# Optimization experiments

Measured on AMD Instinct MI355X. Metric: run time of the kernel, lower is better.

The kernel has to match this reference:

```python
import jax, jax.numpy as jnp
import numpy as np
from jax import lax

B = 1024          # batch_size
T = 20            # timesteps == input_timesteps
IN_DIM = 13       # data_in_dims
OUT_DIM = 9       # data_out_dims
SU = 32           # input_units == output_units (story / weight dim)
H = 32            # LowerRNN hidden_size
INFER_LR = 0.1
INFER_ITERS = 20
L2_LAMBDA = 1e-4
B1, B2, EPS = 0.9, 0.999, 1e-8  # torch.optim.Adam defaults


def _lin_init(key, fan_in, shape):
    bound = 1.0 / np.sqrt(fan_in)
    return jax.random.uniform(key, shape, jnp.float32, -bound, bound)


def setup_inputs() -> dict:
    key = jax.random.key(0)
    ks = jax.random.split(key, 20)
    return {
        "temporal_batch_input": jax.random.normal(ks[0], (T, B, IN_DIM), jnp.float32),
        "temporal_batch_output": jax.random.uniform(ks[1], (T, B, OUT_DIM), jnp.float32),
        # hypernet: 32 -> 128 -> 256 -> 256 -> 32 (ReLU between, linear out)
        "hW1": _lin_init(ks[2], SU, (SU, 128)),   "hb1": _lin_init(ks[3], SU, (128,)),
        "hW2": _lin_init(ks[4], 128, (128, 256)), "hb2": _lin_init(ks[5], 128, (256,)),
        "hW3": _lin_init(ks[6], 256, (256, 256)), "hb3": _lin_init(ks[7], 256, (256,)),
        "hW4": _lin_init(ks[8], 256, (256, SU)),  "hb4": _lin_init(ks[9], 256, (SU,)),
        # LowerRNN: tanh RNN, input 45 = cat(x:13, weights:32)
        "Wih": _lin_init(ks[10], H, (H, IN_DIM + SU)),
        "Whh": _lin_init(ks[11], H, (H, H)),
        "bih": _lin_init(ks[12], H, (H,)),
        "bhh": _lin_init(ks[13], H, (H,)),
        # decoder: Linear(32 -> 9), ReLU applied after
        "Wd": _lin_init(ks[14], H, (H, OUT_DIM)),
        "bd": _lin_init(ks[15], H, (OUT_DIM,)),
    }


def reference(temporal_batch_input, temporal_batch_output,
              hW1, hb1, hW2, hb2, hW3, hb3, hW4, hb4,
              Wih, Whh, bih, bhh, Wd, bd):
    def hyper(s):  # [B,32] -> [B,32]
        h = jax.nn.relu(s @ hW1 + hb1)
        h = jax.nn.relu(h @ hW2 + hb2)
        h = jax.nn.relu(h @ hW3 + hb3)
        return h @ hW4 + hb4

    def rnn_cell(x, h):  # torch nn.RNN tanh cell
        return jnp.tanh(x @ Wih.T + bih + h @ Whh.T + bhh)

    def infer_loss(story, x_t, y_t, hidden):
        w = hyper(story)
        h_new = rnn_cell(jnp.concatenate([x_t, w], axis=1), hidden)
        pred = jax.nn.relu(h_new @ Wd + bd)                       # [B,9]
        err = jnp.mean(jnp.sum((y_t - pred) ** 2, axis=-1))       # batch_errors
        loss = (err
                + jnp.sum(jnp.var(story, axis=0, ddof=1))         # torch.var unbiased
                + L2_LAMBDA * jnp.mean(jnp.sum(story ** 2, axis=-1)))
        return loss, h_new

    grad_fn = jax.grad(infer_loss, has_aux=True)

    def timestep(story, xy):
        # fresh Adam state + fresh hidden every outer timestep (new optimizer each call)
        x_t, y_t = xy
        def adam_iter(carry, i):
            s, m, v, h = carry
            g, h_new = grad_fn(s, x_t, y_t, h)   # hidden is detached in torch -> constant here
            t = (i + 1).astype(s.dtype)
            m = B1 * m + (1.0 - B1) * g
            v = B2 * v + (1.0 - B2) * g * g
            mhat = m / (1.0 - B1 ** t)
            vhat = v / (1.0 - B2 ** t)
            s = s - INFER_LR * mhat / (jnp.sqrt(vhat) + EPS)
            return (s, m, v, h_new), None
        z = jnp.zeros_like(story)
        h0 = jnp.zeros((story.shape[0], H), story.dtype)
        (story, _, _, _), _ = lax.scan(adam_iter, (story, z, z, h0), jnp.arange(INFER_ITERS))
        return story, None

    story0 = jnp.zeros((B, SU), jnp.float32)
    higher, _ = lax.scan(timestep, story0, (temporal_batch_input, temporal_batch_output))
    higher = lax.stop_gradient(higher)  # story is .clone().detach() in torch

    cluster_centers = jnp.mean(higher, axis=0)  # [32]
    w = hyper(higher)                           # [B,32], broadcast over T (repeat)

    def seq_step(h, x_t):
        h = rnn_cell(jnp.concatenate([x_t, w], axis=1), h)
        return h, h
    _, hs = lax.scan(seq_step, jnp.zeros((B, H), jnp.float32), temporal_batch_input)
    preds = jax.nn.relu(hs @ Wd + bd)           # [T,B,9]
    errors = jnp.mean(jnp.sum((preds - temporal_batch_output) ** 2, axis=(0, 2)))
    return errors, cluster_centers
```

## Files before the change

### kernel.cpp

```cpp
#include <hip/hip_runtime.h>

#define NB 256
#define NT 512

constexpr int BATCH = 1024;
constexpr int TSTEPS = 20;
constexpr int IND = 13;
constexpr int OD = 9;
constexpr int SU = 32;
constexpr int HID = 32;
constexpr int ITERS = 20;
constexpr float LR = 0.1f;
constexpr float AB1 = 0.9f;
constexpr float AB2 = 0.999f;
constexpr float AEPS = 1e-8f;

constexpr unsigned SPIN_CAP = 1u << 27;

constexpr size_t OFF_CNT   = 0;
constexpr size_t OFF_ERRP  = 3072;
constexpr size_t OFF_PART  = 4096;
constexpr size_t OFF_WIHT  = 69632;
constexpr size_t OFF_WHHT  = 75392;
constexpr size_t OFF_W2T   = 79488;
constexpr size_t OFF_W3T   = 210560;
constexpr size_t OFF_W4T   = 472704;
constexpr size_t WS_NEEDED = 505472;

__device__ __forceinline__ float ld_coh_f32(const float* p) {
  return __hip_atomic_load(p, __ATOMIC_RELAXED, __HIP_MEMORY_SCOPE_AGENT);
}
__device__ __forceinline__ void st_coh_f32(float* p, float v) {
  __hip_atomic_store(p, v, __ATOMIC_RELAXED, __HIP_MEMORY_SCOPE_AGENT);
}

__device__ __forceinline__ void fma4(float4& a, const float4 w, const float h) {
  a.x += w.x * h; a.y += w.y * h; a.z += w.z * h; a.w += w.w * h;
}
__device__ __forceinline__ float dot4(const float4 a, const float4 b) {
  return a.x * b.x + a.y * b.y + a.z * b.z + a.w * b.w;
}

__global__ void prep_kernel(const float* __restrict__ Wih,
                            const float* __restrict__ Whh,
                            const float* __restrict__ W2,
                            const float* __restrict__ W3,
                            const float* __restrict__ W4,
                            char* __restrict__ ws) {
  float* WihT = reinterpret_cast<float*>(ws + OFF_WIHT);
  float* WhhT = reinterpret_cast<float*>(ws + OFF_WHHT);
  float* W2T  = reinterpret_cast<float*>(ws + OFF_W2T);
  float* W3T  = reinterpret_cast<float*>(ws + OFF_W3T);
  float* W4T  = reinterpret_cast<float*>(ws + OFF_W4T);
  int tid = blockIdx.x * blockDim.x + threadIdx.x;
  int nt = gridDim.x * blockDim.x;
  for (int idx = tid; idx < 32 * 45; idx += nt) {
    int i = idx / 45, c = idx % 45;
    WihT[c * 32 + i] = Wih[idx];
  }
  for (int idx = tid; idx < 32 * 32; idx += nt) {
    int i = idx >> 5, j = idx & 31;
    WhhT[j * 32 + i] = Whh[idx];
  }
  for (int idx = tid; idx < 256 * 128; idx += nt) {
    int k = idx >> 7, j = idx & 127;
    W2T[idx] = W2[j * 256 + k];
  }
  for (int idx = tid; idx < 256 * 256; idx += nt) {
    int k = idx >> 8, j = idx & 255;
    W3T[idx] = W3[j * 256 + k];
  }
  for (int idx = tid; idx < 32 * 256; idx += nt) {
    int k = idx >> 8, j = idx & 255;
    W4T[idx] = W4[j * 32 + k];
  }
}

__global__ __launch_bounds__(NT) void emb_kernel(
    const float* __restrict__ X, const float* __restrict__ Y,
    const float* __restrict__ pW1, const float* __restrict__ pb1,
    const float* __restrict__ pW2, const float* __restrict__ pb2,
    const float* __restrict__ pW3, const float* __restrict__ pb3,
    const float* __restrict__ pW4, const float* __restrict__ pb4,
    const float* __restrict__ pWih, const float* __restrict__ pWhh,
    const float* __restrict__ pbih, const float* __restrict__ pbhh,
    const float* __restrict__ pWd, const float* __restrict__ pbd,
    char* __restrict__ ws, float* __restrict__ out) {
  const int tid = threadIdx.x;
  const int bid = blockIdx.x;
  const int row0 = bid * 4;

  unsigned* cnt  = reinterpret_cast<unsigned*>(ws + OFF_CNT);
  float* errp = reinterpret_cast<float*>(ws + OFF_ERRP);
  float* part = reinterpret_cast<float*>(ws + OFF_PART);
  const float* WihT = reinterpret_cast<const float*>(ws + OFF_WIHT);
  const float* WhhT = reinterpret_cast<const float*>(ws + OFF_WHHT);
  const float* W2T  = reinterpret_cast<const float*>(ws + OFF_W2T);
  const float* W3T  = reinterpret_cast<const float*>(ws + OFF_W3T);
  const float* W4T  = reinterpret_cast<const float*>(ws + OFF_W4T);

  __shared__ alignas(16) float s[4][SU];
  __shared__ alignas(16) float mAd[4][SU];
  __shared__ alignas(16) float vAd[4][SU];
  __shared__ alignas(16) float hOld[4][HID];
  __shared__ alignas(16) float hNew[4][HID];
  __shared__ alignas(16) float h1[4][128];
  __shared__ alignas(16) float h2[4][256];
  __shared__ alignas(16) float h3[4][256];
  __shared__ alignas(16) float wv[4][SU];
  __shared__ alignas(16) float da[4][HID];
  __shared__ alignas(16) float dwb[4][SU];
  __shared__ alignas(16) float dsb[4][SU];
  __shared__ alignas(16) float red2[8192];
  __shared__ float xs[4][IND];
  __shared__ float ysd[4][OD];
  __shared__ float dadec[4][OD];
  __shared__ float mu[SU];
  __shared__ float red[8][SU];

  auto spin_ge = [&](unsigned* cntp, unsigned tgt) {
    unsigned n = 0;
    while (__hip_atomic_load(cntp, __ATOMIC_RELAXED,
                             __HIP_MEMORY_SCOPE_AGENT) < tgt) {
      __builtin_amdgcn_s_sleep(1);
      if (++n >= SPIN_CAP) break;
    }
  };


  auto fwd_l1 = [&]() {
    if (tid < 256) {
      int j0 = (tid & 31) * 4, kg = tid >> 5;
      float4 a0 = {0,0,0,0}, a1 = a0, a2 = a0, a3 = a0;
#pragma unroll
      for (int q = 0; q < 4; ++q) {
        int k = kg * 4 + q;
        float4 w = *reinterpret_cast<const float4*>(pW1 + k * 128 + j0);
        fma4(a0, w, s[0][k]); fma4(a1, w, s[1][k]);
        fma4(a2, w, s[2][k]); fma4(a3, w, s[3][k]);
      }
      *reinterpret_cast<float4*>(&red2[(kg * 4 + 0) * 128 + j0]) = a0;
      *reinterpret_cast<float4*>(&red2[(kg * 4 + 1) * 128 + j0]) = a1;
      *reinterpret_cast<float4*>(&red2[(kg * 4 + 2) * 128 + j0]) = a2;
      *reinterpret_cast<float4*>(&red2[(kg * 4 + 3) * 128 + j0]) = a3;
    }
    __syncthreads();
    int r = tid >> 7, j = tid & 127;
    float sum = pb1[j];
#pragma unroll
    for (int g = 0; g < 8; ++g) sum += red2[(g * 4 + r) * 128 + j];
    h1[r][j] = fmaxf(sum, 0.f);
  };

  auto fwd_wide = [&](const float* __restrict__ W, const float* __restrict__ bias,
                      const float* hin, int K, float* hout) {
    {
      int j0 = (tid & 63) * 4, kg = tid >> 6;
      int kn = K >> 3;
      float4 a0 = {0,0,0,0}, a1 = a0, a2 = a0, a3 = a0;
#pragma unroll 8
      for (int q = 0; q < kn; ++q) {
        int k = kg * kn + q;
        float4 w = *reinterpret_cast<const float4*>(W + k * 256 + j0);
        fma4(a0, w, hin[0 * K + k]); fma4(a1, w, hin[1 * K + k]);
        fma4(a2, w, hin[2 * K + k]); fma4(a3, w, hin[3 * K + k]);
      }
      *reinterpret_cast<float4*>(&red2[(kg * 4 + 0) * 256 + j0]) = a0;
      *reinterpret_cast<float4*>(&red2[(kg * 4 + 1) * 256 + j0]) = a1;
      *reinterpret_cast<float4*>(&red2[(kg * 4 + 2) * 256 + j0]) = a2;
      *reinterpret_cast<float4*>(&red2[(kg * 4 + 3) * 256 + j0]) = a3;
    }
    __syncthreads();
    int o = tid * 2, r = o >> 8, j = o & 255;
    float s0 = bias[j], s1 = bias[j + 1];
#pragma unroll
    for (int g = 0; g < 8; ++g) {
      float2 p = *reinterpret_cast<const float2*>(&red2[(g * 4 + r) * 256 + j]);
      s0 += p.x; s1 += p.y;
    }
    hout[r * 256 + j]     = fmaxf(s0, 0.f);
    hout[r * 256 + j + 1] = fmaxf(s1, 0.f);
  };

  auto fwd_l4 = [&]() {
    if (tid < 128) {
      int j0 = (tid & 7) * 4, kg = tid >> 3;
      float4 a0 = {0,0,0,0}, a1 = a0, a2 = a0, a3 = a0;
#pragma unroll 8
      for (int q = 0; q < 16; ++q) {
        int k = kg * 16 + q;
        float4 w = *reinterpret_cast<const float4*>(pW4 + k * 32 + j0);
        fma4(a0, w, h3[0][k]); fma4(a1, w, h3[1][k]);
        fma4(a2, w, h3[2][k]); fma4(a3, w, h3[3][k]);
      }
      *reinterpret_cast<float4*>(&red2[(kg * 4 + 0) * 32 + j0]) = a0;
      *reinterpret_cast<float4*>(&red2[(kg * 4 + 1) * 32 + j0]) = a1;
      *reinterpret_cast<float4*>(&red2[(kg * 4 + 2) * 32 + j0]) = a2;
      *reinterpret_cast<float4*>(&red2[(kg * 4 + 3) * 32 + j0]) = a3;
    }
    __syncthreads();
    if (tid < 128) {
      int r = tid >> 5, j = tid & 31;
      float sum = pb4[j];
#pragma unroll
      for (int g = 0; g < 16; ++g) sum += red2[(g * 4 + r) * 32 + j];
      wv[r][j] = sum;
    }
  };

  auto rnn_fwd = [&]() {
    if (tid < 128) {
      int r = tid >> 5, i = tid & 31;
      float a = pbih[i] + pbhh[i];
#pragma unroll
      for (int c = 0; c < IND; ++c) a += xs[r][c] * WihT[c * 32 + i];
#pragma unroll 8
      for (int c = 0; c < SU; ++c) a += wv[r][c] * WihT[(13 + c) * 32 + i];
#pragma unroll 8
      for (int j = 0; j < HID; ++j) a += hOld[r][j] * WhhT[j * 32 + i];
      hNew[r][i] = tanhf(a);
    }
  };

  auto bwdT256 = [&](const float* __restrict__ WT, const float* din, int Kd,
                     float* dmask) {
    {
      int j0 = (tid & 63) * 4, kg = tid >> 6;
      int kn = Kd >> 3;
      float4 a0 = {0,0,0,0}, a1 = a0, a2 = a0, a3 = a0;
#pragma unroll 4
      for (int q = 0; q < kn; ++q) {
        int k = kg * kn + q;
        float4 w = *reinterpret_cast<const float4*>(WT + k * 256 + j0);
        fma4(a0, w, din[0 * Kd + k]); fma4(a1, w, din[1 * Kd + k]);
        fma4(a2, w, din[2 * Kd + k]); fma4(a3, w, din[3 * Kd + k]);
      }
      *reinterpret_cast<float4*>(&red2[(kg * 4 + 0) * 256 + j0]) = a0;
      *reinterpret_cast<float4*>(&red2[(kg * 4 + 1) * 256 + j0]) = a1;
      *reinterpret_cast<float4*>(&red2[(kg * 4 + 2) * 256 + j0]) = a2;
      *reinterpret_cast<float4*>(&red2[(kg * 4 + 3) * 256 + j0]) = a3;
    }
    __syncthreads();
    int o = tid * 2, r = o >> 8, j = o & 255;
    float s0 = 0.f, s1 = 0.f;
#pragma unroll
    for (int g = 0; g < 8; ++g) {
      float2 p = *reinterpret_cast<const float2*>(&red2[(g * 4 + r) * 256 + j]);
      s0 += p.x; s1 += p.y;
    }
    float m0 = dmask[r * 256 + j], m1 = dmask[r * 256 + j + 1];
    dmask[r * 256 + j]     = (m0 > 0.f) ? s0 : 0.f;
    dmask[r * 256 + j + 1] = (m1 > 0.f) ? s1 : 0.f;
  };

  auto bwd_dh1 = [&]() {
    {
      int j0 = (tid & 31) * 4, kg = tid >> 5;
      float4 a0 = {0,0,0,0}, a1 = a0, a2 = a0, a3 = a0;
#pragma unroll 8
      for (int q = 0; q < 16; ++q) {
        int k = kg * 16 + q;
        float4 w = *reinterpret_cast<const float4*>(W2T + k * 128 + j0);
        fma4(a0, w, h2[0][k]); fma4(a1, w, h2[1][k]);
        fma4(a2, w, h2[2][k]); fma4(a3, w, h2[3][k]);
      }
      *reinterpret_cast<float4*>(&red2[(kg * 4 + 0) * 128 + j0]) = a0;
      *reinterpret_cast<float4*>(&red2[(kg * 4 + 1) * 128 + j0]) = a1;
      *reinterpret_cast<float4*>(&red2[(kg * 4 + 2) * 128 + j0]) = a2;
      *reinterpret_cast<float4*>(&red2[(kg * 4 + 3) * 128 + j0]) = a3;
    }
    __syncthreads();
    int r = tid >> 7, j = tid & 127;
    float sum = 0.f;
#pragma unroll
    for (int g = 0; g < 16; ++g) sum += red2[(g * 4 + r) * 128 + j];
    h1[r][j] = (h1[r][j] > 0.f) ? sum : 0.f;
  };

  auto bwd_ds = [&]() {
    if (tid < 256) {
      int k0 = (tid & 7) * 4, jg = (tid >> 3) & 31;
      int j0 = jg * 4;
      float4 g0 = *reinterpret_cast<const float4*>(&h1[0][j0]);
      float4 g1 = *reinterpret_cast<const float4*>(&h1[1][j0]);
      float4 g2 = *reinterpret_cast<const float4*>(&h1[2][j0]);
      float4 g3 = *reinterpret_cast<const float4*>(&h1[3][j0]);
      float4 a0, a1, a2, a3;
      float* A0 = &a0.x; float* A1 = &a1.x; float* A2 = &a2.x; float* A3 = &a3.x;
#pragma unroll
      for (int q = 0; q < 4; ++q) {
        int k = k0 + q;
        float4 w = *reinterpret_cast<const float4*>(pW1 + k * 128 + j0);
        A0[q] = dot4(w, g0); A1[q] = dot4(w, g1);
        A2[q] = dot4(w, g2); A3[q] = dot4(w, g3);
      }
      *reinterpret_cast<float4*>(&red2[jg * 128 + 0 * 32 + k0]) = a0;
      *reinterpret_cast<float4*>(&red2[jg * 128 + 1 * 32 + k0]) = a1;
      *reinterpret_cast<float4*>(&red2[jg * 128 + 2 * 32 + k0]) = a2;
      *reinterpret_cast<float4*>(&red2[jg * 128 + 3 * 32 + k0]) = a3;
    }
    __syncthreads();
    if (tid < 128) {
      int r = tid >> 5, k = tid & 31;
      float sum = 0.f;
#pragma unroll
      for (int g = 0; g < 32; ++g) sum += red2[g * 128 + r * 32 + k];
      dsb[r][k] = sum;
    }
  };

  auto publish = [&](int pslot) {
    __syncthreads();
    if (tid < SU) {
      st_coh_f32(&part[(size_t)pslot * NB * SU + (size_t)bid * SU + tid],
                 s[0][tid] + s[1][tid] + s[2][tid] + s[3][tid]);
    }
    if (tid == 0)
      __hip_atomic_fetch_add(&cnt[pslot], 1u, __ATOMIC_RELEASE,
                             __HIP_MEMORY_SCOPE_AGENT);
  };

  if (tid < 128) { int r = tid >> 5, c = tid & 31; s[r][c] = 0.f; }
  publish(0);

  for (int ts = 0; ts < TSTEPS; ++ts) {
    if (tid < 4 * IND) {
      int r = tid / IND, c = tid % IND;
      xs[r][c] = X[(size_t)ts * BATCH * IND + (size_t)(row0 + r) * IND + c];
    }
    if (tid >= 64 && tid < 64 + 4 * OD) {
      int q = tid - 64; int r = q / OD, c = q % OD;
      ysd[r][c] = Y[(size_t)ts * BATCH * OD + (size_t)(row0 + r) * OD + c];
    }
    if (tid >= 128 && tid < 256) {
      int q = tid - 128; int r = q >> 5, c = q & 31;
      mAd[r][c] = 0.f; vAd[r][c] = 0.f; hOld[r][c] = 0.f;
    }
    float pb1t = 1.f, pb2t = 1.f;

    for (int it = 0; it < ITERS; ++it) {
      const int gi = ts * ITERS + it;
      const int p = gi & 1;
      pb1t *= AB1; pb2t *= AB2;

      if (tid == 0) spin_ge(&cnt[p], (unsigned)(gi / 2 + 1) * (unsigned)NB);
      __syncthreads();

      if (tid < 256) {
        int c = tid & 31, grp = tid >> 5;
        const float* P = part + (size_t)p * NB * SU;
        float sum = 0.f;
#pragma unroll 8
        for (int b2 = grp * 32; b2 < grp * 32 + 32; ++b2)
          sum += ld_coh_f32(&P[b2 * SU + c]);
        red[grp][c] = sum;
      }
      __syncthreads();
      if (tid < SU) {
        float sum = 0.f;
#pragma unroll
        for (int g2 = 0; g2 < 8; ++g2) sum += red[g2][tid];
        mu[tid] = sum * (1.f / 1024.f);
      }
      __syncthreads();

      fwd_l1(); __syncthreads();
      fwd_wide(pW2, pb2, &h1[0][0], 128, &h2[0][0]); __syncthreads();
      fwd_wide(pW3, pb3, &h2[0][0], 256, &h3[0][0]); __syncthreads();
      fwd_l4(); __syncthreads();
      rnn_fwd(); __syncthreads();

      if (tid < 36) {
        int r = tid / OD, d = tid % OD;
        float adec = pbd[d];
#pragma unroll
        for (int i = 0; i < HID; ++i) adec += hNew[r][i] * pWd[i * OD + d];
        float pr = fmaxf(adec, 0.f);
        dadec[r][d] = (adec > 0.f) ? (2.f / 1024.f) * (pr - ysd[r][d]) : 0.f;
      }
      __syncthreads();

      if (tid < 128) {
        int r = tid >> 5, i = tid & 31;
        float t1 = 0.f;
#pragma unroll
        for (int d = 0; d < OD; ++d) t1 += dadec[r][d] * pWd[i * OD + d];
        float hn = hNew[r][i];
        da[r][i] = t1 * (1.f - hn * hn);
      }
      __syncthreads();

      if (tid < 128) {
        int r = tid >> 5, k = tid & 31;
        float t2 = 0.f;
#pragma unroll 8
        for (int i = 0; i < HID; ++i) t2 += da[r][i] * WihT[(13 + k) * 32 + i];
        dwb[r][k] = t2;
      }
      __syncthreads();

      bwdT256(W4T, &dwb[0][0], 32, &h3[0][0]); __syncthreads();
      bwdT256(W3T, &h3[0][0], 256, &h2[0][0]); __syncthreads();
      bwd_dh1(); __syncthreads();
      bwd_ds(); __syncthreads();

      if (tid < 128) {
        int r = tid >> 5, c = tid & 31;
        float sv = s[r][c];
        float g = dsb[r][c] + (sv - mu[c]) * (2.f / 1023.f) + sv * (2e-4f / 1024.f);
        float m2 = AB1 * mAd[r][c] + (1.f - AB1) * g;
        float v2 = AB2 * vAd[r][c] + (1.f - AB2) * g * g;
        mAd[r][c] = m2; vAd[r][c] = v2;
        float mh = m2 / (1.f - pb1t);
        float vh = v2 / (1.f - pb2t);
        s[r][c] = sv - LR * mh / (sqrtf(vh) + AEPS);
        hOld[r][c] = hNew[r][c];
      }

      publish((gi + 1) & 1);
    }
  }

  fwd_l1(); __syncthreads();
  fwd_wide(pW2, pb2, &h1[0][0], 128, &h2[0][0]); __syncthreads();
  fwd_wide(pW3, pb3, &h2[0][0], 256, &h3[0][0]); __syncthreads();
  fwd_l4(); __syncthreads();

  if (tid < 128) { int r = tid >> 5, i = tid & 31; hOld[r][i] = 0.f; }
  __syncthreads();

  float errACC = 0.f;
  for (int t2 = 0; t2 < TSTEPS; ++t2) {
    if (tid < 4 * IND) {
      int r = tid / IND, c = tid % IND;
      xs[r][c] = X[(size_t)t2 * BATCH * IND + (size_t)(row0 + r) * IND + c];
    }
    __syncthreads();
    rnn_fwd(); __syncthreads();
    if (tid < 36) {
      int r = tid / OD, d = tid % OD;
      float adec = pbd[d];
#pragma unroll
      for (int i = 0; i < HID; ++i) adec += hNew[r][i] * pWd[i * OD + d];
      float pr = fmaxf(adec, 0.f);
      float e = pr - Y[(size_t)t2 * BATCH * OD + (size_t)(row0 + r) * OD + d];
      errACC += e * e;
    }
    if (tid < 128) { int r = tid >> 5, i = tid & 31; hOld[r][i] = hNew[r][i]; }
    __syncthreads();
  }

  if (tid < 36) (&red[0][0])[tid] = errACC;
  __syncthreads();
  if (tid == 0) {
    float sum = 0.f;
    for (int q = 0; q < 36; ++q) sum += (&red[0][0])[q];
    st_coh_f32(&errp[bid], sum);
    __hip_atomic_fetch_add(&cnt[2], 1u, __ATOMIC_RELEASE,
                           __HIP_MEMORY_SCOPE_AGENT);
  }

  if (bid == 0) {
    if (tid == 0) {
      spin_ge(&cnt[2], (unsigned)NB);
      spin_ge(&cnt[0], (unsigned)(TSTEPS * ITERS / 2 + 1) * (unsigned)NB);
    }
    __syncthreads();
    if (tid == 0) {
      float sum = 0.f;
      for (int b = 0; b < NB; ++b) sum += ld_coh_f32(&errp[b]);
      out[0] = sum * (1.f / 1024.f);
    }
    if (tid >= 64 && tid < 96) {
      int c = tid - 64;
      float sum = 0.f;
      for (int b = 0; b < NB; ++b)
        sum += ld_coh_f32(&part[(size_t)b * SU + c]);
      out[1 + c] = sum * (1.f / 1024.f);
    }
  }
}

extern "C" void kernel_launch(void* const* d_in, const int* in_sizes, int n_in,
                              void* d_out, int out_size, void* d_ws, size_t ws_size,
                              hipStream_t stream) {
  (void)in_sizes; (void)n_in; (void)out_size;
  if (ws_size < WS_NEEDED) return;

  const float* X   = (const float*)d_in[0];
  const float* Y   = (const float*)d_in[1];
  const float* W1  = (const float*)d_in[2];
  const float* b1  = (const float*)d_in[3];
  const float* W2  = (const float*)d_in[4];
  const float* b2  = (const float*)d_in[5];
  const float* W3  = (const float*)d_in[6];
  const float* b3  = (const float*)d_in[7];
  const float* W4  = (const float*)d_in[8];
  const float* b4  = (const float*)d_in[9];
  const float* Wih = (const float*)d_in[10];
  const float* Whh = (const float*)d_in[11];
  const float* bih = (const float*)d_in[12];
  const float* bhh = (const float*)d_in[13];
  const float* Wd  = (const float*)d_in[14];
  const float* bd  = (const float*)d_in[15];

  hipMemsetAsync(d_ws, 0, 3072, stream);
  prep_kernel<<<128, 256, 0, stream>>>(Wih, Whh, W2, W3, W4, (char*)d_ws);
  emb_kernel<<<NB, NT, 0, stream>>>(X, Y, W1, b1, W2, b2, W3, b3, W4, b4,
                                    Wih, Whh, bih, bhh, Wd, bd,
                                    (char*)d_ws, (float*)d_out);
}
```

Baseline: 16.20 ms.

## Double threads per block and defer grid barrier until after local backprop

Raises block size from 512 to 1024 threads. Each half of the block now handles two of the four batch rows in the hypernet forward and backward matmuls, so the work per thread is halved. It also moves the spin-wait on the cross-block partial sums, and the mean reduction over those sums, from the start of each Adam iteration to just before the update step. The mean is only needed there, so the barrier latency can overlap the per-block forward and backward compute. The risks are higher register pressure under the 1024-thread launch bound and a larger reduction buffer in shared memory.

```diff
diff --git a/kernel.cpp b/kernel.cpp
--- a/kernel.cpp
+++ b/kernel.cpp
@@ -1,7 +1,7 @@
 #include <hip/hip_runtime.h>
 
 #define NB 256
-#define NT 512
+#define NT 1024
 
 constexpr int BATCH = 1024;
 constexpr int TSTEPS = 20;
@@ -89,8 +89,10 @@
   const int tid = threadIdx.x;
   const int bid = blockIdx.x;
   const int row0 = bid * 4;
-
-  unsigned* cnt  = reinterpret_cast<unsigned*>(ws + OFF_CNT);
+  const int t  = tid & 511;
+  const int rA = (tid >> 9) * 2, rB = rA + 1;
+
+  unsigned* cnt = reinterpret_cast<unsigned*>(ws + OFF_CNT);
   float* errp = reinterpret_cast<float*>(ws + OFF_ERRP);
   float* part = reinterpret_cast<float*>(ws + OFF_PART);
   const float* WihT = reinterpret_cast<const float*>(ws + OFF_WIHT);
@@ -115,8 +117,7 @@
   __shared__ float xs[4][IND];
   __shared__ float ysd[4][OD];
   __shared__ float dadec[4][OD];
-  __shared__ float mu[SU];
-  __shared__ float red[8][SU];
+  __shared__ float red[32][SU];
 
   auto spin_ge = [&](unsigned* cntp, unsigned tgt) {
     unsigned n = 0;
@@ -129,74 +130,65 @@
 
 
   auto fwd_l1 = [&]() {
-    if (tid < 256) {
-      int j0 = (tid & 31) * 4, kg = tid >> 5;
-      float4 a0 = {0,0,0,0}, a1 = a0, a2 = a0, a3 = a0;
+    if (t < 256) {
+      int j0 = (t & 31) * 4, kg = t >> 5;
+      float4 aA = {0,0,0,0}, aB = aA;
 #pragma unroll
       for (int q = 0; q < 4; ++q) {
         int k = kg * 4 + q;
         float4 w = *reinterpret_cast<const float4*>(pW1 + k * 128 + j0);
-        fma4(a0, w, s[0][k]); fma4(a1, w, s[1][k]);
-        fma4(a2, w, s[2][k]); fma4(a3, w, s[3][k]);
-      }
-      *reinterpret_cast<float4*>(&red2[(kg * 4 + 0) * 128 + j0]) = a0;
-      *reinterpret_cast<float4*>(&red2[(kg * 4 + 1) * 128 + j0]) = a1;
-      *reinterpret_cast<float4*>(&red2[(kg * 4 + 2) * 128 + j0]) = a2;
-      *reinterpret_cast<float4*>(&red2[(kg * 4 + 3) * 128 + j0]) = a3;
-    }
-    __syncthreads();
-    int r = tid >> 7, j = tid & 127;
-    float sum = pb1[j];
-#pragma unroll
-    for (int g = 0; g < 8; ++g) sum += red2[(g * 4 + r) * 128 + j];
-    h1[r][j] = fmaxf(sum, 0.f);
+        fma4(aA, w, s[rA][k]); fma4(aB, w, s[rB][k]);
+      }
+      *reinterpret_cast<float4*>(&red2[(kg * 4 + rA) * 128 + j0]) = aA;
+      *reinterpret_cast<float4*>(&red2[(kg * 4 + rB) * 128 + j0]) = aB;
+    }
+    __syncthreads();
+    if (tid < 512) {
+      int r = tid >> 7, j = tid & 127;
+      float sum = pb1[j];
+#pragma unroll
+      for (int g = 0; g < 8; ++g) sum += red2[(g * 4 + r) * 128 + j];
+      h1[r][j] = fmaxf(sum, 0.f);
+    }
   };
 
   auto fwd_wide = [&](const float* __restrict__ W, const float* __restrict__ bias,
                       const float* hin, int K, float* hout) {
     {
-      int j0 = (tid & 63) * 4, kg = tid >> 6;
+      int j0 = (t & 63) * 4, kg = t >> 6;
       int kn = K >> 3;
-      float4 a0 = {0,0,0,0}, a1 = a0, a2 = a0, a3 = a0;
+      float4 aA = {0,0,0,0}, aB = aA;
 #pragma unroll 8
       for (int q = 0; q < kn; ++q) {
         int k = kg * kn + q;
         float4 w = *reinterpret_cast<const float4*>(W + k * 256 + j0);
-        fma4(a0, w, hin[0 * K + k]); fma4(a1, w, hin[1 * K + k]);
-        fma4(a2, w, hin[2 * K + k]); fma4(a3, w, hin[3 * K + k]);
-      }
-      *reinterpret_cast<float4*>(&red2[(kg * 4 + 0) * 256 + j0]) = a0;
-      *reinterpret_cast<float4*>(&red2[(kg * 4 + 1) * 256 + j0]) = a1;
-      *reinterpret_cast<float4*>(&red2[(kg * 4 + 2) * 256 + j0]) = a2;
-      *reinterpret_cast<float4*>(&red2[(kg * 4 + 3) * 256 + j0]) = a3;
-    }
-    __syncthreads();
-    int o = tid * 2, r = o >> 8, j = o & 255;
-    float s0 = bias[j], s1 = bias[j + 1];
-#pragma unroll
-    for (int g = 0; g < 8; ++g) {
-      float2 p = *reinterpret_cast<const float2*>(&red2[(g * 4 + r) * 256 + j]);
-      s0 += p.x; s1 += p.y;
-    }
-    hout[r * 256 + j]     = fmaxf(s0, 0.f);
-    hout[r * 256 + j + 1] = fmaxf(s1, 0.f);
+        fma4(aA, w, hin[rA * K + k]); fma4(aB, w, hin[rB * K + k]);
+      }
+      *reinterpret_cast<float4*>(&red2[(kg * 4 + rA) * 256 + j0]) = aA;
+      *reinterpret_cast<float4*>(&red2[(kg * 4 + rB) * 256 + j0]) = aB;
+    }
+    __syncthreads();
+    {
+      int r = tid >> 8, j = tid & 255;
+      float s0 = bias[j];
+#pragma unroll
+      for (int g = 0; g < 8; ++g) s0 += red2[(g * 4 + r) * 256 + j];
+      hout[r * 256 + j] = fmaxf(s0, 0.f);
+    }
   };
 
   auto fwd_l4 = [&]() {
-    if (tid < 128) {
-      int j0 = (tid & 7) * 4, kg = tid >> 3;
-      float4 a0 = {0,0,0,0}, a1 = a0, a2 = a0, a3 = a0;
+    if (t < 128) {
+      int j0 = (t & 7) * 4, kg = t >> 3;
+      float4 aA = {0,0,0,0}, aB = aA;
 #pragma unroll 8
       for (int q = 0; q < 16; ++q) {
         int k = kg * 16 + q;
         float4 w = *reinterpret_cast<const float4*>(pW4 + k * 32 + j0);
-        fma4(a0, w, h3[0][k]); fma4(a1, w, h3[1][k]);
-        fma4(a2, w, h3[2][k]); fma4(a3, w, h3[3][k]);
-      }
-      *reinterpret_cast<float4*>(&red2[(kg * 4 + 0) * 32 + j0]) = a0;
-      *reinterpret_cast<float4*>(&red2[(kg * 4 + 1) * 32 + j0]) = a1;
-      *reinterpret_cast<float4*>(&red2[(kg * 4 + 2) * 32 + j0]) = a2;
-      *reinterpret_cast<float4*>(&red2[(kg * 4 + 3) * 32 + j0]) = a3;
+        fma4(aA, w, h3[rA][k]); fma4(aB, w, h3[rB][k]);
+      }
+      *reinterpret_cast<float4*>(&red2[(kg * 4 + rA) * 32 + j0]) = aA;
+      *reinterpret_cast<float4*>(&red2[(kg * 4 + rB) * 32 + j0]) = aB;
     }
     __syncthreads();
     if (tid < 128) {
@@ -225,79 +217,68 @@
   auto bwdT256 = [&](const float* __restrict__ WT, const float* din, int Kd,
                      float* dmask) {
     {
-      int j0 = (tid & 63) * 4, kg = tid >> 6;
+      int j0 = (t & 63) * 4, kg = t >> 6;
       int kn = Kd >> 3;
-      float4 a0 = {0,0,0,0}, a1 = a0, a2 = a0, a3 = a0;
+      float4 aA = {0,0,0,0}, aB = aA;
 #pragma unroll 4
       for (int q = 0; q < kn; ++q) {
         int k = kg * kn + q;
         float4 w = *reinterpret_cast<const float4*>(WT + k * 256 + j0);
-        fma4(a0, w, din[0 * Kd + k]); fma4(a1, w, din[1 * Kd + k]);
-        fma4(a2, w, din[2 * Kd + k]); fma4(a3, w, din[3 * Kd + k]);
-      }
-      *reinterpret_cast<float4*>(&red2[(kg * 4 + 0) * 256 + j0]) = a0;
-      *reinterpret_cast<float4*>(&red2[(kg * 4 + 1) * 256 + j0]) = a1;
-      *reinterpret_cast<float4*>(&red2[(kg * 4 + 2) * 256 + j0]) = a2;
-      *reinterpret_cast<float4*>(&red2[(kg * 4 + 3) * 256 + j0]) = a3;
-    }
-    __syncthreads();
-    int o = tid * 2, r = o >> 8, j = o & 255;
-    float s0 = 0.f, s1 = 0.f;
-#pragma unroll
-    for (int g = 0; g < 8; ++g) {
-      float2 p = *reinterpret_cast<const float2*>(&red2[(g * 4 + r) * 256 + j]);
-      s0 += p.x; s1 += p.y;
-    }
-    float m0 = dmask[r * 256 + j], m1 = dmask[r * 256 + j + 1];
-    dmask[r * 256 + j]     = (m0 > 0.f) ? s0 : 0.f;
-    dmask[r * 256 + j + 1] = (m1 > 0.f) ? s1 : 0.f;
+        fma4(aA, w, din[rA * Kd + k]); fma4(aB, w, din[rB * Kd + k]);
+      }
+      *reinterpret_cast<float4*>(&red2[(kg * 4 + rA) * 256 + j0]) = aA;
+      *reinterpret_cast<float4*>(&red2[(kg * 4 + rB) * 256 + j0]) = aB;
+    }
+    __syncthreads();
+    {
+      int r = tid >> 8, j = tid & 255;
+      float s0 = 0.f;
+#pragma unroll
+      for (int g = 0; g < 8; ++g) s0 += red2[(g * 4 + r) * 256 + j];
+      float m0 = dmask[r * 256 + j];
+      dmask[r * 256 + j] = (m0 > 0.f) ? s0 : 0.f;
+    }
   };
 
   auto bwd_dh1 = [&]() {
     {
-      int j0 = (tid & 31) * 4, kg = tid >> 5;
-      float4 a0 = {0,0,0,0}, a1 = a0, a2 = a0, a3 = a0;
+      int j0 = (t & 31) * 4, kg = t >> 5;
+      float4 aA = {0,0,0,0}, aB = aA;
 #pragma unroll 8
       for (int q = 0; q < 16; ++q) {
         int k = kg * 16 + q;
         float4 w = *reinterpret_cast<const float4*>(W2T + k * 128 + j0);
-        fma4(a0, w, h2[0][k]); fma4(a1, w, h2[1][k]);
-        fma4(a2, w, h2[2][k]); fma4(a3, w, h2[3][k]);
-      }
-      *reinterpret_cast<float4*>(&red2[(kg * 4 + 0) * 128 + j0]) = a0;
-      *reinterpret_cast<float4*>(&red2[(kg * 4 + 1) * 128 + j0]) = a1;
-      *reinterpret_cast<float4*>(&red2[(kg * 4 + 2) * 128 + j0]) = a2;
-      *reinterpret_cast<float4*>(&red2[(kg * 4 + 3) * 128 + j0]) = a3;
-    }
-    __syncthreads();
-    int r = tid >> 7, j = tid & 127;
-    float sum = 0.f;
-#pragma unroll
-    for (int g = 0; g < 16; ++g) sum += red2[(g * 4 + r) * 128 + j];
-    h1[r][j] = (h1[r][j] > 0.f) ? sum : 0.f;
+        fma4(aA, w, h2[rA][k]); fma4(aB, w, h2[rB][k]);
+      }
+      *reinterpret_cast<float4*>(&red2[(kg * 4 + rA) * 128 + j0]) = aA;
+      *reinterpret_cast<float4*>(&red2[(kg * 4 + rB) * 128 + j0]) = aB;
+    }
+    __syncthreads();
+    if (tid < 512) {
+      int r = tid >> 7, j = tid & 127;
+      float sum = 0.f;
+#pragma unroll
+      for (int g = 0; g < 16; ++g) sum += red2[(g * 4 + r) * 128 + j];
+      h1[r][j] = (h1[r][j] > 0.f) ? sum : 0.f;
+    }
   };
 
   auto bwd_ds = [&]() {
-    if (tid < 256) {
-      int k0 = (tid & 7) * 4, jg = (tid >> 3) & 31;
+    if (t < 256) {
+      int k0 = (t & 7) * 4, jg = t >> 3;
       int j0 = jg * 4;
-      float4 g0 = *reinterpret_cast<const float4*>(&h1[0][j0]);
-      float4 g1 = *reinterpret_cast<const float4*>(&h1[1][j0]);
-      float4 g2 = *reinterpret_cast<const float4*>(&h1[2][j0]);
-      float4 g3 = *reinterpret_cast<const float4*>(&h1[3][j0]);
-      float4 a0, a1, a2, a3;
-      float* A0 = &a0.x; float* A1 = &a1.x; float* A2 = &a2.x; float* A3 = &a3.x;
+      float4 gA = *reinterpret_cast<const float4*>(&h1[rA][j0]);
+      float4 gB = *reinterpret_cast<const float4*>(&h1[rB][j0]);
+      float4 aA, aB;
+      float* A = &aA.x; float* Bp = &aB.x;
 #pragma unroll
       for (int q = 0; q < 4; ++q) {
         int k = k0 + q;
         float4 w = *reinterpret_cast<const float4*>(pW1 + k * 128 + j0);
-        A0[q] = dot4(w, g0); A1[q] = dot4(w, g1);
-        A2[q] = dot4(w, g2); A3[q] = dot4(w, g3);
-      }
-      *reinterpret_cast<float4*>(&red2[jg * 128 + 0 * 32 + k0]) = a0;
-      *reinterpret_cast<float4*>(&red2[jg * 128 + 1 * 32 + k0]) = a1;
-      *reinterpret_cast<float4*>(&red2[jg * 128 + 2 * 32 + k0]) = a2;
-      *reinterpret_cast<float4*>(&red2[jg * 128 + 3 * 32 + k0]) = a3;
+        A[q] = dot4(w, gA); Bp[q] = dot4(w, gB);
+      }
+      *reinterpret_cast<float4*>(&red2[jg * 128 + rA * 32 + k0]) = aA;
+      *reinterpret_cast<float4*>(&red2[jg * 128 + rB * 32 + k0]) = aB;
     }
     __syncthreads();
     if (tid < 128) {
@@ -342,27 +323,6 @@
       const int gi = ts * ITERS + it;
       const int p = gi & 1;
       pb1t *= AB1; pb2t *= AB2;
-
-      if (tid == 0) spin_ge(&cnt[p], (unsigned)(gi / 2 + 1) * (unsigned)NB);
-      __syncthreads();
-
-      if (tid < 256) {
-        int c = tid & 31, grp = tid >> 5;
-        const float* P = part + (size_t)p * NB * SU;
-        float sum = 0.f;
-#pragma unroll 8
-        for (int b2 = grp * 32; b2 < grp * 32 + 32; ++b2)
-          sum += ld_coh_f32(&P[b2 * SU + c]);
-        red[grp][c] = sum;
-      }
-      __syncthreads();
-      if (tid < SU) {
-        float sum = 0.f;
-#pragma unroll
-        for (int g2 = 0; g2 < 8; ++g2) sum += red[g2][tid];
-        mu[tid] = sum * (1.f / 1024.f);
-      }
-      __syncthreads();
 
       fwd_l1(); __syncthreads();
       fwd_wide(pW2, pb2, &h1[0][0], 128, &h2[0][0]); __syncthreads();
@@ -404,10 +364,28 @@
       bwd_dh1(); __syncthreads();
       bwd_ds(); __syncthreads();
 
+      if (tid == 0) spin_ge(&cnt[p], (unsigned)(gi / 2 + 1) * (unsigned)NB);
+      __syncthreads();
+
+      {
+        int c = tid & 31, grp = tid >> 5;
+        const float* P = part + (size_t)p * NB * SU;
+        float sum = 0.f;
+#pragma unroll
+        for (int b2 = grp * 8; b2 < grp * 8 + 8; ++b2)
+          sum += ld_coh_f32(&P[b2 * SU + c]);
+        red[grp][c] = sum;
+      }
+      __syncthreads();
+
       if (tid < 128) {
         int r = tid >> 5, c = tid & 31;
+        float msum = 0.f;
+#pragma unroll
+        for (int g = 0; g < 32; ++g) msum += red[g][c];
+        float muc = msum * (1.f / 1024.f);
         float sv = s[r][c];
-        float g = dsb[r][c] + (sv - mu[c]) * (2.f / 1023.f) + sv * (2e-4f / 1024.f);
+        float g = dsb[r][c] + (sv - muc) * (2.f / 1023.f) + sv * (2e-4f / 1024.f);
         float m2 = AB1 * mAd[r][c] + (1.f - AB1) * g;
         float v2 = AB2 * vAd[r][c] + (1.f - AB2) * g * g;
         mAd[r][c] = m2; vAd[r][c] = v2;
```

Result: faster. 13.26 ms (-18.1%).
